# Optimization experiments

Hardware: AMD Instinct MI355X
Metric: run time of the kernel (lower is better)

The kernel has to match this reference:

```python
import jax, jax.numpy as jnp
import numpy as np

B, N, M = 2, 16200, 128
DIM, QK_DIM, HEADS, GS = 256, 256, 8, 128


def setup_inputs() -> dict:
    key = jax.random.key(0)
    ks = jax.random.split(key, 10)
    sorted_x = jax.random.normal(ks[0], (B, N, DIM), dtype=jnp.float32)
    prototypes = jax.random.normal(ks[1], (B, M, DIM), dtype=jnp.float32)
    # idx_last must be a per-batch permutation of 0..N-1 (scatter-back to original order)
    idx_last = jnp.argsort(jax.random.uniform(ks[2], (B, N)), axis=-1).astype(jnp.int32)[..., None]
    s = 0.02
    Wq = jax.random.normal(ks[3], (DIM, QK_DIM), dtype=jnp.float32) * s
    Wk = jax.random.normal(ks[4], (DIM, QK_DIM), dtype=jnp.float32) * s
    Wv = jax.random.normal(ks[5], (DIM, DIM), dtype=jnp.float32) * s
    Wpk = jax.random.normal(ks[6], (DIM, QK_DIM), dtype=jnp.float32) * s
    Wpv = jax.random.normal(ks[7], (DIM, DIM), dtype=jnp.float32) * s
    Wproj = jax.random.normal(ks[8], (DIM, DIM), dtype=jnp.float32) * s
    return {"sorted_x": sorted_x, "idx_last": idx_last, "prototypes": prototypes,
            "Wq": Wq, "Wk": Wk, "Wv": Wv, "Wpk": Wpk, "Wpv": Wpv, "Wproj": Wproj}


def _iasa(sorted_x, idx_last, prototypes, Wq, Wk, Wv, Wpk, Wpv, Wproj):
    b, n, dim = sorted_x.shape
    h = HEADS
    gs = min(n, GS)
    ng = (n + gs - 1) // gs
    pad_n = ng * gs - n
    dq = Wq.shape[1] // h   # qk head dim
    dv = Wv.shape[1] // h   # v head dim
    scale = 1.0 / jnp.sqrt(jnp.asarray(dq, sorted_x.dtype))

    q = sorted_x @ Wq
    k = sorted_x @ Wk
    v = sorted_x @ Wv

    # pad q with flipped tail (pad_n tokens) -> [b, ng*gs, qk]
    q_pad = jnp.concatenate([q, q[:, n - pad_n:n][:, ::-1]], axis=1)
    qh = q_pad.reshape(b, ng, gs, h, dq).transpose(0, 1, 3, 2, 4)  # b ng h gs d

    def windows(t, c):
        # pad with flipped last (pad_n + gs) tokens -> length (ng+1)*gs, then
        # overlapping windows of 2*gs with stride gs (== torch unfold)
        t_pad = jnp.concatenate([t, t[:, n - pad_n - gs:n][:, ::-1]], axis=1)
        tr = t_pad.reshape(b, ng + 1, gs, c)
        win = jnp.concatenate([tr[:, :-1], tr[:, 1:]], axis=2)  # b ng 2gs c
        return win.reshape(b, ng, 2 * gs, h, c // h).transpose(0, 1, 3, 2, 4)  # b ng h 2gs d

    kw = windows(k, Wk.shape[1])
    vw = windows(v, Wv.shape[1])

    # local overlapping-window attention
    a1 = jax.nn.softmax(jnp.einsum('bghqd,bghkd->bghqk', qh, kw) * scale, axis=-1)
    o1 = jnp.einsum('bghqk,bghkd->bghqd', a1, vw)

    # global prototype cross-attention
    kg = (prototypes @ Wpk).reshape(b, -1, h, dq).transpose(0, 2, 1, 3)  # b h m d
    vg = (prototypes @ Wpv).reshape(b, -1, h, dv).transpose(0, 2, 1, 3)
    a2 = jax.nn.softmax(jnp.einsum('bghqd,bhmd->bghqm', qh, kg) * scale, axis=-1)
    o2 = jnp.einsum('bghqm,bhmd->bghqd', a2, vg)

    out = (o1 + o2).transpose(0, 1, 3, 2, 4).reshape(b, ng * gs, h * dv)[:, :n]

    # scatter back to original order: result[b, idx[b,i], c] = out[b, i, c]
    idx = jnp.broadcast_to(idx_last, out.shape)
    b_idx = jnp.arange(b)[:, None, None]
    c_idx = jnp.arange(out.shape[-1])[None, None, :]
    out = out.at[b_idx, idx, c_idx].set(out)
    return out @ Wproj


def reference(sorted_x, idx_last, prototypes, Wq, Wk, Wv, Wpk, Wpv, Wproj):
    return _iasa(sorted_x, idx_last, prototypes, Wq, Wk, Wv, Wpk, Wpv, Wproj)
```

## Files before the change

kernel.cpp:

```cpp
#include <hip/hip_runtime.h>


typedef unsigned short u16;
typedef unsigned int   u32;
typedef __attribute__((ext_vector_type(8))) u16   u16x8;
typedef __attribute__((ext_vector_type(4))) u16   u16x4;
typedef __attribute__((ext_vector_type(8))) short bf16x8;
typedef __attribute__((ext_vector_type(4))) float f32x4;

#define NB   2
#define NN   16200
#define MM   128
#define NH   8
#define NGRP 127
#define APAD 72

static __device__ __forceinline__ u16 f2bf(float f) {
  u32 u = __float_as_uint(f);
  return (u16)((u + 0x7FFFu + ((u >> 16) & 1u)) >> 16);
}

static __device__ __forceinline__ f32x4 mfma16(bf16x8 a, bf16x8 b, f32x4 c) {
  return __builtin_amdgcn_mfma_f32_16x16x32_bf16(a, b, c, 0, 0, 0);
}

__global__ void prep_wt(const float* __restrict__ w0, const float* __restrict__ w1,
                        const float* __restrict__ w2, const float* __restrict__ w3,
                        const float* __restrict__ w4, const float* __restrict__ w5,
                        u16* __restrict__ wt) {
  int m = blockIdx.y;
  const float* W = m == 0 ? w0 : m == 1 ? w1 : m == 2 ? w2 : m == 3 ? w3 : m == 4 ? w4 : w5;
  int t = blockIdx.x * 256 + threadIdx.x;
  int o = t >> 8, i = t & 255;
  wt[((size_t)(m * 256 + o) << 8) + i] = f2bf(W[(i << 8) + o]);
}

template <bool AF32, bool CF32>
__global__ __launch_bounds__(256) void gemm_bt(
    const void* __restrict__ Av, int numRows,
    const u16* __restrict__ Bt,
    void* __restrict__ Cv, int ldc,
    const int* __restrict__ idx)
{
  __shared__ __attribute__((aligned(16))) u16 sA[128 * APAD];
  __shared__ __attribute__((aligned(16))) u16 sB[128 * APAD];
  int rowBase = blockIdx.x << 7;
  int colBase = blockIdx.y << 7;
  int tid = threadIdx.x;
  int lane = tid & 63, w = tid >> 6;
  int wr = (w >> 1) << 6, wc = (w & 1) << 6;
  int lr = lane & 15, lg = lane >> 4;

  f32x4 acc[4][4];
#pragma unroll
  for (int i = 0; i < 4; ++i)
#pragma unroll
    for (int j = 0; j < 4; ++j) acc[i][j] = (f32x4)0.0f;

  for (int kt = 0; kt < 4; ++kt) {
#pragma unroll
    for (int i = 0; i < 4; ++i) {
      int e = tid + (i << 8);
      int r = e >> 3;
      int cc = (e & 7) << 3;
      int gr = rowBase + r;
      gr = gr < numRows ? gr : 0;
      if constexpr (AF32) {
        const float* A = (const float*)Av;
        f32x4 a0 = *(const f32x4*)(A + ((size_t)gr << 8) + (kt << 6) + cc);
        f32x4 a1 = *(const f32x4*)(A + ((size_t)gr << 8) + (kt << 6) + cc + 4);
        u16x8 val;
#pragma unroll
        for (int j = 0; j < 4; ++j) { val[j] = f2bf(a0[j]); val[4 + j] = f2bf(a1[j]); }
        *(u16x8*)(sA + r * APAD + cc) = val;
      } else {
        const u16* A = (const u16*)Av;
        *(u16x8*)(sA + r * APAD + cc) =
            *(const u16x8*)(A + ((size_t)gr << 8) + (kt << 6) + cc);
      }
      *(u16x8*)(sB + r * APAD + cc) =
          *(const u16x8*)(Bt + ((size_t)(colBase + r) << 8) + (kt << 6) + cc);
    }
    __syncthreads();
#pragma unroll
    for (int kk = 0; kk < 2; ++kk) {
      bf16x8 af[4], bfv[4];
#pragma unroll
      for (int m = 0; m < 4; ++m)
        af[m] = *(const bf16x8*)(sA + (wr + (m << 4) + lr) * APAD + (kk << 5) + (lg << 3));
#pragma unroll
      for (int n = 0; n < 4; ++n)
        bfv[n] = *(const bf16x8*)(sB + (wc + (n << 4) + lr) * APAD + (kk << 5) + (lg << 3));
#pragma unroll
      for (int m = 0; m < 4; ++m)
#pragma unroll
        for (int n = 0; n < 4; ++n) acc[m][n] = mfma16(af[m], bfv[n], acc[m][n]);
    }
    __syncthreads();
  }

#pragma unroll
  for (int m = 0; m < 4; ++m) {
    int row0 = rowBase + wr + (m << 4) + (lg << 2);
#pragma unroll
    for (int r = 0; r < 4; ++r) {
      int rr = row0 + r;
      if (rr >= numRows) continue;
      size_t orow = rr;
      if (idx) {
        int b = rr / NN;
        orow = (size_t)b * NN + idx[rr];
      }
#pragma unroll
      for (int n = 0; n < 4; ++n) {
        int col = colBase + wc + (n << 4) + lr;
        if constexpr (CF32) {
          ((float*)Cv)[orow * ldc + col] = acc[m][n][r];
        } else {
          ((u16*)Cv)[orow * ldc + col] = f2bf(acc[m][n][r]);
        }
      }
    }
  }
}

__global__ __launch_bounds__(256) void attn_kernel(
    const u16* __restrict__ qkv,
    const u16* __restrict__ kgvg,
    u16* __restrict__ outa)
{
  __shared__ __attribute__((aligned(16))) u16 sKV[8448];
  __shared__ __attribute__((aligned(16))) u16 sVgt[32 * 136];
  __shared__ __attribute__((aligned(16))) u16 sP[4][16 * 264];

  int bid = blockIdx.x;
  int qh = bid & 1;
  int rest = bid >> 1;
  int g = rest % NGRP;
  int h = (rest / NGRP) & 7;
  int b = rest / (NGRP * NH);

  int tid = threadIdx.x, lane = tid & 63, w = tid >> 6;
  int lr = lane & 15, lg = lane >> 4;

  const size_t bOff = (size_t)b * NN * 768;
  const int hoff = h << 5;
  const int kbase = g << 7;

#pragma unroll
  for (int i = 0; i < 4; ++i) {
    int e = tid + (i << 8);
    int r = e >> 2, c = (e & 3) << 3;
    int kp = kbase + r;
    int tok = kp < NN ? kp : 2 * NN - 1 - kp;
    *(u16x8*)(sKV + (r << 5) + c) =
        *(const u16x8*)(qkv + bOff + (size_t)tok * 768 + 256 + hoff + c);
  }
#pragma unroll
  for (int i = 0; i < 2; ++i) {
    int e = tid + (i << 8);
    int r = e >> 2, c = (e & 3) << 3;
    u16x8 v = *(const u16x8*)(kgvg + ((size_t)(b * MM + r) << 9) + 256 + hoff + c);
#pragma unroll
    for (int u = 0; u < 8; ++u) sVgt[(c + u) * 136 + r] = v[u];
  }
  __syncthreads();

  const float scale = 0.17677669529663687f;
  int qrow = (qh << 6) + (w << 4) + lr;
  int qtok = kbase + qrow;
  qtok = qtok < NN ? qtok : 2 * NN - 1 - qtok;
  bf16x8 qf = *(const bf16x8*)(qkv + bOff + (size_t)qtok * 768 + hoff + (lg << 3));

  f32x4 z = (f32x4)0.0f;
  f32x4 s[16];
#pragma unroll
  for (int kt = 0; kt < 16; ++kt) {
    bf16x8 kf = *(const bf16x8*)(sKV + (((kt << 4) + lr) << 5) + (lg << 3));
    s[kt] = mfma16(kf, qf, z);
  }
  float mx = -1e30f;
#pragma unroll
  for (int kt = 0; kt < 16; ++kt)
    mx = fmaxf(mx, fmaxf(fmaxf(s[kt][0], s[kt][1]), fmaxf(s[kt][2], s[kt][3])));
  mx = fmaxf(mx, __shfl_xor(mx, 16, 64));
  mx = fmaxf(mx, __shfl_xor(mx, 32, 64));
  float sum = 0.f;
#pragma unroll
  for (int kt = 0; kt < 16; ++kt)
#pragma unroll
    for (int r = 0; r < 4; ++r) {
      float p = __expf((s[kt][r] - mx) * scale);
      s[kt][r] = p;
      sum += p;
    }
  sum += __shfl_xor(sum, 16, 64);
  sum += __shfl_xor(sum, 32, 64);
  float inv = 1.0f / sum;
#pragma unroll
  for (int kt = 0; kt < 16; ++kt) {
    u16x4 pk;
#pragma unroll
    for (int r = 0; r < 4; ++r) pk[r] = f2bf(s[kt][r] * inv);
    *(u16x4*)(&sP[w][lr * 264 + (kt << 4) + (lg << 2)]) = pk;
  }
  __syncthreads();

#pragma unroll
  for (int i = 0; i < 4; ++i) {
    int e = tid + (i << 8);
    int r = e >> 2, c = (e & 3) << 3;
    int kp = kbase + r;
    int tok = kp < NN ? kp : 2 * NN - 1 - kp;
    u16x8 v = *(const u16x8*)(qkv + bOff + (size_t)tok * 768 + 512 + hoff + c);
#pragma unroll
    for (int u = 0; u < 8; ++u) sKV[(c + u) * 264 + r] = v[u];
  }
  __syncthreads();

  f32x4 o0 = z, o1 = z;
#pragma unroll
  for (int kb = 0; kb < 8; ++kb) {
    bf16x8 pf = *(const bf16x8*)(&sP[w][lr * 264 + (kb << 5) + (lg << 3)]);
    bf16x8 v0 = *(const bf16x8*)(sKV + lr * 264 + (kb << 5) + (lg << 3));
    bf16x8 v1 = *(const bf16x8*)(sKV + (16 + lr) * 264 + (kb << 5) + (lg << 3));
    o0 = mfma16(v0, pf, o0);
    o1 = mfma16(v1, pf, o1);
  }

  f32x4 sg[8];
#pragma unroll
  for (int kt = 0; kt < 8; ++kt) {
    bf16x8 kf = *(const bf16x8*)(kgvg + ((size_t)(b * MM + (kt << 4) + lr) << 9) + hoff + (lg << 3));
    sg[kt] = mfma16(kf, qf, z);
  }
  float mx2 = -1e30f;
#pragma unroll
  for (int kt = 0; kt < 8; ++kt)
    mx2 = fmaxf(mx2, fmaxf(fmaxf(sg[kt][0], sg[kt][1]), fmaxf(sg[kt][2], sg[kt][3])));
  mx2 = fmaxf(mx2, __shfl_xor(mx2, 16, 64));
  mx2 = fmaxf(mx2, __shfl_xor(mx2, 32, 64));
  float sum2 = 0.f;
#pragma unroll
  for (int kt = 0; kt < 8; ++kt)
#pragma unroll
    for (int r = 0; r < 4; ++r) {
      float p = __expf((sg[kt][r] - mx2) * scale);
      sg[kt][r] = p;
      sum2 += p;
    }
  sum2 += __shfl_xor(sum2, 16, 64);
  sum2 += __shfl_xor(sum2, 32, 64);
  float inv2 = 1.0f / sum2;
#pragma unroll
  for (int kt = 0; kt < 8; ++kt) {
    u16x4 pk;
#pragma unroll
    for (int r = 0; r < 4; ++r) pk[r] = f2bf(sg[kt][r] * inv2);
    *(u16x4*)(&sP[w][lr * 264 + (kt << 4) + (lg << 2)]) = pk;
  }
#pragma unroll
  for (int kb = 0; kb < 4; ++kb) {
    bf16x8 pf = *(const bf16x8*)(&sP[w][lr * 264 + (kb << 5) + (lg << 3)]);
    bf16x8 v0 = *(const bf16x8*)(sVgt + lr * 136 + (kb << 5) + (lg << 3));
    bf16x8 v1 = *(const bf16x8*)(sVgt + (16 + lr) * 136 + (kb << 5) + (lg << 3));
    o0 = mfma16(v0, pf, o0);
    o1 = mfma16(v1, pf, o1);
  }

  int token = kbase + (qh << 6) + (w << 4) + lr;
  if (token < NN) {
    size_t base = ((size_t)b * NN + token) * 256 + hoff;
    u16x4 w0v, w1v;
#pragma unroll
    for (int r = 0; r < 4; ++r) {
      w0v[r] = f2bf(o0[r]);
      w1v[r] = f2bf(o1[r]);
    }
    *(u16x4*)(outa + base + (lg << 2)) = w0v;
    *(u16x4*)(outa + base + 16 + (lg << 2)) = w1v;
  }
}

extern "C" void kernel_launch(void* const* d_in, const int* in_sizes, int n_in,
                              void* d_out, int out_size, void* d_ws, size_t ws_size,
                              hipStream_t stream) {
  const float* x     = (const float*)d_in[0];
  const int*   idx   = (const int*)d_in[1];
  const float* proto = (const float*)d_in[2];
  const float* Wq    = (const float*)d_in[3];
  const float* Wk    = (const float*)d_in[4];
  const float* Wv    = (const float*)d_in[5];
  const float* Wpk   = (const float*)d_in[6];
  const float* Wpv   = (const float*)d_in[7];
  const float* Wproj = (const float*)d_in[8];

  u16* wt   = (u16*)d_ws;
  u16* qkv  = wt + (size_t)1536 * 256;
  u16* kgvg = qkv + (size_t)32400 * 768;
  u16* attn = kgvg + (size_t)256 * 512;

  prep_wt<<<dim3(256, 6), 256, 0, stream>>>(Wq, Wk, Wv, Wpk, Wpv, Wproj, wt);
  gemm_bt<true, false><<<dim3(254, 6), 256, 0, stream>>>(x, NB * NN, wt, qkv, 768, nullptr);
  gemm_bt<true, false><<<dim3(2, 4), 256, 0, stream>>>(proto, NB * MM, wt + (size_t)768 * 256,
                                                       kgvg, 512, nullptr);
  attn_kernel<<<dim3(NB * NH * NGRP * 2), 256, 0, stream>>>(qkv, kgvg, attn);
  gemm_bt<false, true><<<dim3(254, 2), 256, 0, stream>>>(attn, NB * NN, wt + (size_t)1280 * 256,
                                                         d_out, 256, idx);
}
```

Before: 221.9 us.

## Process both query halves per block and swizzle transposed V in LDS

Each attention block now handles all 128 query rows of a group instead of 64, so the K/V window and prototype V are loaded into shared memory once and shared by two query passes. The block count is halved to match. The K tile row stride is padded to 40, and the transposed V and prototype V stores use an XOR swizzle to cut LDS bank conflicts on both writes and reads. In exchange each block does twice the work, holds more score registers (two sets of 16 accumulators), and the grid has half as many blocks, which may lower occupancy and parallelism.

```diff
diff --git a/kernel.cpp b/kernel.cpp
--- a/kernel.cpp
+++ b/kernel.cpp
@@ -129,16 +129,14 @@
     const u16* __restrict__ kgvg,
     u16* __restrict__ outa)
 {
-  __shared__ __attribute__((aligned(16))) u16 sKV[8448];
+  __shared__ __attribute__((aligned(16))) u16 sKV[256 * 40];
   __shared__ __attribute__((aligned(16))) u16 sVgt[32 * 136];
   __shared__ __attribute__((aligned(16))) u16 sP[4][16 * 264];
 
   int bid = blockIdx.x;
-  int qh = bid & 1;
-  int rest = bid >> 1;
-  int g = rest % NGRP;
-  int h = (rest / NGRP) & 7;
-  int b = rest / (NGRP * NH);
+  int g = bid % NGRP;
+  int h = (bid / NGRP) & 7;
+  int b = bid / (NGRP * NH);
 
   int tid = threadIdx.x, lane = tid & 63, w = tid >> 6;
   int lr = lane & 15, lg = lane >> 4;
@@ -153,7 +151,7 @@
     int r = e >> 2, c = (e & 3) << 3;
     int kp = kbase + r;
     int tok = kp < NN ? kp : 2 * NN - 1 - kp;
-    *(u16x8*)(sKV + (r << 5) + c) =
+    *(u16x8*)(sKV + r * 40 + c) =
         *(const u16x8*)(qkv + bOff + (size_t)tok * 768 + 256 + hoff + c);
   }
 #pragma unroll
@@ -162,47 +160,26 @@
     int r = e >> 2, c = (e & 3) << 3;
     u16x8 v = *(const u16x8*)(kgvg + ((size_t)(b * MM + r) << 9) + 256 + hoff + c);
 #pragma unroll
-    for (int u = 0; u < 8; ++u) sVgt[(c + u) * 136 + r] = v[u];
+    for (int u = 0; u < 8; ++u) {
+      int dv = c + u;
+      sVgt[dv * 136 + (r ^ ((((dv >> 3) & 3)) << 3))] = v[u];
+    }
   }
   __syncthreads();
 
   const float scale = 0.17677669529663687f;
-  int qrow = (qh << 6) + (w << 4) + lr;
-  int qtok = kbase + qrow;
-  qtok = qtok < NN ? qtok : 2 * NN - 1 - qtok;
-  bf16x8 qf = *(const bf16x8*)(qkv + bOff + (size_t)qtok * 768 + hoff + (lg << 3));
+  int qt0 = kbase + (w << 4) + lr;       qt0 = qt0 < NN ? qt0 : 2 * NN - 1 - qt0;
+  int qt1 = kbase + 64 + (w << 4) + lr;  qt1 = qt1 < NN ? qt1 : 2 * NN - 1 - qt1;
+  bf16x8 qf0 = *(const bf16x8*)(qkv + bOff + (size_t)qt0 * 768 + hoff + (lg << 3));
+  bf16x8 qf1 = *(const bf16x8*)(qkv + bOff + (size_t)qt1 * 768 + hoff + (lg << 3));
 
   f32x4 z = (f32x4)0.0f;
-  f32x4 s[16];
+  f32x4 s0[16], s1[16];
 #pragma unroll
   for (int kt = 0; kt < 16; ++kt) {
-    bf16x8 kf = *(const bf16x8*)(sKV + (((kt << 4) + lr) << 5) + (lg << 3));
-    s[kt] = mfma16(kf, qf, z);
-  }
-  float mx = -1e30f;
-#pragma unroll
-  for (int kt = 0; kt < 16; ++kt)
-    mx = fmaxf(mx, fmaxf(fmaxf(s[kt][0], s[kt][1]), fmaxf(s[kt][2], s[kt][3])));
-  mx = fmaxf(mx, __shfl_xor(mx, 16, 64));
-  mx = fmaxf(mx, __shfl_xor(mx, 32, 64));
-  float sum = 0.f;
-#pragma unroll
-  for (int kt = 0; kt < 16; ++kt)
-#pragma unroll
-    for (int r = 0; r < 4; ++r) {
-      float p = __expf((s[kt][r] - mx) * scale);
-      s[kt][r] = p;
-      sum += p;
-    }
-  sum += __shfl_xor(sum, 16, 64);
-  sum += __shfl_xor(sum, 32, 64);
-  float inv = 1.0f / sum;
-#pragma unroll
-  for (int kt = 0; kt < 16; ++kt) {
-    u16x4 pk;
-#pragma unroll
-    for (int r = 0; r < 4; ++r) pk[r] = f2bf(s[kt][r] * inv);
-    *(u16x4*)(&sP[w][lr * 264 + (kt << 4) + (lg << 2)]) = pk;
+    bf16x8 kf = *(const bf16x8*)(sKV + ((kt << 4) + lr) * 40 + (lg << 3));
+    s0[kt] = mfma16(kf, qf0, z);
+    s1[kt] = mfma16(kf, qf1, z);
   }
   __syncthreads();
 
@@ -214,72 +191,107 @@
     int tok = kp < NN ? kp : 2 * NN - 1 - kp;
     u16x8 v = *(const u16x8*)(qkv + bOff + (size_t)tok * 768 + 512 + hoff + c);
 #pragma unroll
-    for (int u = 0; u < 8; ++u) sKV[(c + u) * 264 + r] = v[u];
+    for (int u = 0; u < 8; ++u) {
+      int dv = c + u;
+      sKV[dv * 264 + (r ^ ((((dv >> 3) & 3)) << 3))] = v[u];
+    }
   }
   __syncthreads();
 
-  f32x4 o0 = z, o1 = z;
-#pragma unroll
-  for (int kb = 0; kb < 8; ++kb) {
-    bf16x8 pf = *(const bf16x8*)(&sP[w][lr * 264 + (kb << 5) + (lg << 3)]);
-    bf16x8 v0 = *(const bf16x8*)(sKV + lr * 264 + (kb << 5) + (lg << 3));
-    bf16x8 v1 = *(const bf16x8*)(sKV + (16 + lr) * 264 + (kb << 5) + (lg << 3));
-    o0 = mfma16(v0, pf, o0);
-    o1 = mfma16(v1, pf, o1);
-  }
-
-  f32x4 sg[8];
-#pragma unroll
-  for (int kt = 0; kt < 8; ++kt) {
-    bf16x8 kf = *(const bf16x8*)(kgvg + ((size_t)(b * MM + (kt << 4) + lr) << 9) + hoff + (lg << 3));
-    sg[kt] = mfma16(kf, qf, z);
-  }
-  float mx2 = -1e30f;
-#pragma unroll
-  for (int kt = 0; kt < 8; ++kt)
-    mx2 = fmaxf(mx2, fmaxf(fmaxf(sg[kt][0], sg[kt][1]), fmaxf(sg[kt][2], sg[kt][3])));
-  mx2 = fmaxf(mx2, __shfl_xor(mx2, 16, 64));
-  mx2 = fmaxf(mx2, __shfl_xor(mx2, 32, 64));
-  float sum2 = 0.f;
-#pragma unroll
-  for (int kt = 0; kt < 8; ++kt)
-#pragma unroll
-    for (int r = 0; r < 4; ++r) {
-      float p = __expf((sg[kt][r] - mx2) * scale);
-      sg[kt][r] = p;
-      sum2 += p;
-    }
-  sum2 += __shfl_xor(sum2, 16, 64);
-  sum2 += __shfl_xor(sum2, 32, 64);
-  float inv2 = 1.0f / sum2;
-#pragma unroll
-  for (int kt = 0; kt < 8; ++kt) {
-    u16x4 pk;
-#pragma unroll
-    for (int r = 0; r < 4; ++r) pk[r] = f2bf(sg[kt][r] * inv2);
-    *(u16x4*)(&sP[w][lr * 264 + (kt << 4) + (lg << 2)]) = pk;
-  }
-#pragma unroll
-  for (int kb = 0; kb < 4; ++kb) {
-    bf16x8 pf = *(const bf16x8*)(&sP[w][lr * 264 + (kb << 5) + (lg << 3)]);
-    bf16x8 v0 = *(const bf16x8*)(sVgt + lr * 136 + (kb << 5) + (lg << 3));
-    bf16x8 v1 = *(const bf16x8*)(sVgt + (16 + lr) * 136 + (kb << 5) + (lg << 3));
-    o0 = mfma16(v0, pf, o0);
-    o1 = mfma16(v1, pf, o1);
-  }
-
-  int token = kbase + (qh << 6) + (w << 4) + lr;
-  if (token < NN) {
-    size_t base = ((size_t)b * NN + token) * 256 + hoff;
-    u16x4 w0v, w1v;
-#pragma unroll
-    for (int r = 0; r < 4; ++r) {
-      w0v[r] = f2bf(o0[r]);
-      w1v[r] = f2bf(o1[r]);
-    }
-    *(u16x4*)(outa + base + (lg << 2)) = w0v;
-    *(u16x4*)(outa + base + 16 + (lg << 2)) = w1v;
-  }
+  const int sw0 = ((lr >> 3) & 3) << 3;
+  const int sw1 = (((16 + lr) >> 3) & 3) << 3;
+
+  auto run_pass = [&](f32x4 (&s)[16], bf16x8 qfp, int pbase) {
+    float mx = -1e30f;
+#pragma unroll
+    for (int kt = 0; kt < 16; ++kt)
+      mx = fmaxf(mx, fmaxf(fmaxf(s[kt][0], s[kt][1]), fmaxf(s[kt][2], s[kt][3])));
+    mx = fmaxf(mx, __shfl_xor(mx, 16, 64));
+    mx = fmaxf(mx, __shfl_xor(mx, 32, 64));
+    float sum = 0.f;
+#pragma unroll
+    for (int kt = 0; kt < 16; ++kt)
+#pragma unroll
+      for (int r = 0; r < 4; ++r) {
+        float p = __expf((s[kt][r] - mx) * scale);
+        s[kt][r] = p;
+        sum += p;
+      }
+    sum += __shfl_xor(sum, 16, 64);
+    sum += __shfl_xor(sum, 32, 64);
+    float inv = 1.0f / sum;
+#pragma unroll
+    for (int kt = 0; kt < 16; ++kt) {
+      u16x4 pk;
+#pragma unroll
+      for (int r = 0; r < 4; ++r) pk[r] = f2bf(s[kt][r] * inv);
+      *(u16x4*)(&sP[w][lr * 264 + (kt << 4) + (lg << 2)]) = pk;
+    }
+    f32x4 o0 = z, o1 = z;
+#pragma unroll
+    for (int kb = 0; kb < 8; ++kb) {
+      int k0 = (kb << 5) + (lg << 3);
+      bf16x8 pf = *(const bf16x8*)(&sP[w][lr * 264 + k0]);
+      bf16x8 v0 = *(const bf16x8*)(sKV + lr * 264 + (k0 ^ sw0));
+      bf16x8 v1 = *(const bf16x8*)(sKV + (16 + lr) * 264 + (k0 ^ sw1));
+      o0 = mfma16(v0, pf, o0);
+      o1 = mfma16(v1, pf, o1);
+    }
+    f32x4 sg[8];
+#pragma unroll
+    for (int kt = 0; kt < 8; ++kt) {
+      bf16x8 kf = *(const bf16x8*)(kgvg + ((size_t)(b * MM + (kt << 4) + lr) << 9) + hoff + (lg << 3));
+      sg[kt] = mfma16(kf, qfp, z);
+    }
+    float mx2 = -1e30f;
+#pragma unroll
+    for (int kt = 0; kt < 8; ++kt)
+      mx2 = fmaxf(mx2, fmaxf(fmaxf(sg[kt][0], sg[kt][1]), fmaxf(sg[kt][2], sg[kt][3])));
+    mx2 = fmaxf(mx2, __shfl_xor(mx2, 16, 64));
+    mx2 = fmaxf(mx2, __shfl_xor(mx2, 32, 64));
+    float sum2 = 0.f;
+#pragma unroll
+    for (int kt = 0; kt < 8; ++kt)
+#pragma unroll
+      for (int r = 0; r < 4; ++r) {
+        float p = __expf((sg[kt][r] - mx2) * scale);
+        sg[kt][r] = p;
+        sum2 += p;
+      }
+    sum2 += __shfl_xor(sum2, 16, 64);
+    sum2 += __shfl_xor(sum2, 32, 64);
+    float inv2 = 1.0f / sum2;
+#pragma unroll
+    for (int kt = 0; kt < 8; ++kt) {
+      u16x4 pk;
+#pragma unroll
+      for (int r = 0; r < 4; ++r) pk[r] = f2bf(sg[kt][r] * inv2);
+      *(u16x4*)(&sP[w][lr * 264 + (kt << 4) + (lg << 2)]) = pk;
+    }
+#pragma unroll
+    for (int kb = 0; kb < 4; ++kb) {
+      int k0 = (kb << 5) + (lg << 3);
+      bf16x8 pf = *(const bf16x8*)(&sP[w][lr * 264 + k0]);
+      bf16x8 v0 = *(const bf16x8*)(sVgt + lr * 136 + (k0 ^ sw0));
+      bf16x8 v1 = *(const bf16x8*)(sVgt + (16 + lr) * 136 + (k0 ^ sw1));
+      o0 = mfma16(v0, pf, o0);
+      o1 = mfma16(v1, pf, o1);
+    }
+    int token = kbase + pbase + (w << 4) + lr;
+    if (token < NN) {
+      size_t base = ((size_t)b * NN + token) * 256 + hoff;
+      u16x4 w0v, w1v;
+#pragma unroll
+      for (int r = 0; r < 4; ++r) {
+        w0v[r] = f2bf(o0[r]);
+        w1v[r] = f2bf(o1[r]);
+      }
+      *(u16x4*)(outa + base + (lg << 2)) = w0v;
+      *(u16x4*)(outa + base + 16 + (lg << 2)) = w1v;
+    }
+  };
+  run_pass(s0, qf0, 0);
+  run_pass(s1, qf1, 64);
 }
 
 extern "C" void kernel_launch(void* const* d_in, const int* in_sizes, int n_in,
@@ -304,7 +316,7 @@
   gemm_bt<true, false><<<dim3(254, 6), 256, 0, stream>>>(x, NB * NN, wt, qkv, 768, nullptr);
   gemm_bt<true, false><<<dim3(2, 4), 256, 0, stream>>>(proto, NB * MM, wt + (size_t)768 * 256,
                                                        kgvg, 512, nullptr);
-  attn_kernel<<<dim3(NB * NH * NGRP * 2), 256, 0, stream>>>(qkv, kgvg, attn);
+  attn_kernel<<<dim3(NB * NH * NGRP), 256, 0, stream>>>(qkv, kgvg, attn);
   gemm_bt<false, true><<<dim3(254, 2), 256, 0, stream>>>(attn, NB * NN, wt + (size_t)1280 * 256,
                                                          d_out, 256, idx);
 }
```

Result: slower. 244.1 us (+10.0%).
